# Optimization experiments

Hardware: AMD Instinct MI355X
Metric: run time of the kernel (lower is better)

The kernel has to match this reference:

```python
import jax, jax.numpy as jnp
import numpy as np

VOCAB, EMB, HID, NCLS = 50257, 48, 128, 2000
B, S = 512, 1024


def setup_inputs() -> dict:
    key = jax.random.key(0)
    ks = jax.random.split(key, 8)
    x = jax.random.randint(ks[0], (B, S), 0, VOCAB)
    emb_table = jax.random.normal(ks[1], (VOCAB, EMB), dtype=jnp.float32)
    emb_table = emb_table.at[0].set(0.0)  # padding_idx=0
    k_ih = 1.0 / np.sqrt(HID)
    w_ih = jax.random.uniform(ks[2], (4 * HID, EMB), minval=-k_ih, maxval=k_ih, dtype=jnp.float32)
    w_hh = jax.random.uniform(ks[3], (4 * HID, HID), minval=-k_ih, maxval=k_ih, dtype=jnp.float32)
    b_ih = jax.random.uniform(ks[4], (4 * HID,), minval=-k_ih, maxval=k_ih, dtype=jnp.float32)
    b_hh = jax.random.uniform(ks[5], (4 * HID,), minval=-k_ih, maxval=k_ih, dtype=jnp.float32)
    k_fc = 1.0 / np.sqrt(HID)
    w_fc = jax.random.uniform(ks[6], (NCLS, HID), minval=-k_fc, maxval=k_fc, dtype=jnp.float32)
    b_fc = jax.random.uniform(ks[7], (NCLS,), minval=-k_fc, maxval=k_fc, dtype=jnp.float32)
    return {"x": x, "emb_table": emb_table, "w_ih": w_ih, "w_hh": w_hh,
            "b_ih": b_ih, "b_hh": b_hh, "w_fc": w_fc, "b_fc": b_fc}


def _lstm_last_hidden(e, w_ih, w_hh, b_ih, b_hh):
    # e: [B, S, E]. Precompute input contributions for all timesteps (one big GEMM).
    xg = jnp.einsum('bse,ge->bsg', e, w_ih) + b_ih + b_hh  # [B, S, 4H]
    xg = jnp.transpose(xg, (1, 0, 2))                      # [S, B, 4H]
    Bn = e.shape[0]
    h0 = jnp.zeros((Bn, HID), e.dtype)
    c0 = jnp.zeros((Bn, HID), e.dtype)

    def step(carry, xg_t):
        h, c = carry
        g = xg_t + h @ w_hh.T                              # [B, 4H]
        i, f, gg, o = jnp.split(g, 4, axis=-1)             # PyTorch gate order i,f,g,o
        i = jax.nn.sigmoid(i)
        f = jax.nn.sigmoid(f)
        gg = jnp.tanh(gg)
        o = jax.nn.sigmoid(o)
        c = f * c + i * gg
        h = o * jnp.tanh(c)
        return (h, c), None

    (h_n, _), _ = jax.lax.scan(step, (h0, c0), xg)
    return h_n


def reference(x, emb_table, w_ih, w_hh, b_ih, b_hh, w_fc, b_fc):
    e = emb_table[x]                                       # [B, S, E] gather
    h_n = _lstm_last_hidden(e, w_ih, w_hh, b_ih, b_hh)     # [B, H]
    return h_n @ w_fc.T + b_fc                             # [B, NCLS]
```

## Files before the change

### kernel.cpp

```cpp
#include <hip/hip_runtime.h>

#define DI __device__ __forceinline__

typedef unsigned int uint;
typedef unsigned short ushort;
typedef _Float16 half2t __attribute__((ext_vector_type(2)));

#define VOCAB 50257
#define NEMB 48
#define HID 128
#define G4 512
#define NCLS 2000
#define BATCH 512
#define SEQ 1024

#if __has_builtin(__builtin_amdgcn_fdot2)
DI float fdot2(half2t a, half2t b, float c) { return __builtin_amdgcn_fdot2(a, b, c, false); }
#else
DI float fdot2(half2t a, half2t b, float c) { return c + (float)a.x * (float)b.x + (float)a.y * (float)b.y; }
#endif

DI float sigm(float x) {
  return __builtin_amdgcn_rcpf(1.0f + __builtin_amdgcn_exp2f(-1.4426950408889634f * x));
}
DI float tanhfast(float x) {
  return 1.0f - 2.0f * __builtin_amdgcn_rcpf(__builtin_amdgcn_exp2f(2.8853900817779268f * x) + 1.0f);
}

#define VROWS 32
__global__ __launch_bounds__(512) void build_P(
    const float* __restrict__ emb, const float* __restrict__ w_ih,
    const float* __restrict__ b_ih, const float* __restrict__ b_hh,
    _Float16* __restrict__ P)
{
  __shared__ __align__(16) float eL[VROWS][NEMB];
  const int tid = threadIdx.x;
  const int v0 = blockIdx.x * VROWS;
  int nrows = VOCAB - v0; if (nrows > VROWS) nrows = VROWS;

  for (int f = tid; f < nrows * NEMB; f += 512)
    eL[f / NEMB][f % NEMB] = emb[(size_t)v0 * NEMB + f];

  float w[NEMB];
  {
    const float* wr = w_ih + (size_t)tid * NEMB;
#pragma unroll
    for (int k = 0; k < NEMB; k++) w[k] = wr[k];
  }
  float bias = b_ih[tid] + b_hh[tid];
  __syncthreads();

  for (int v = 0; v < nrows; v++) {
    const float4* e4 = (const float4*)&eL[v][0];
    float a = bias;
#pragma unroll
    for (int k = 0; k < NEMB / 4; k++) {
      float4 e = e4[k];
      a += w[4 * k] * e.x + w[4 * k + 1] * e.y + w[4 * k + 2] * e.z + w[4 * k + 3] * e.w;
    }
    P[(size_t)(v0 + v) * G4 + tid] = (_Float16)a;
  }
}

template<bool USE_P>
__global__ __launch_bounds__(256, 2) void lstm_scan(
    const int* __restrict__ x, const float* __restrict__ emb,
    const float* __restrict__ w_ih, const float* __restrict__ w_hh,
    const float* __restrict__ b_ih, const float* __restrict__ b_hh,
    const _Float16* __restrict__ P, float* __restrict__ hout)
{
  __shared__ int tokL[SEQ];
  __shared__ __align__(16) _Float16 h16[HID];
  __shared__ float g32[G4];
  __shared__ __align__(8) half2t e16[2][NEMB / 2];

  const int tid = threadIdx.x;
  const int b = blockIdx.x;

  {
    const int* xp = x + (size_t)b * SEQ;
#pragma unroll
    for (int i = 0; i < SEQ / 256; i++) tokL[tid + 256 * i] = xp[tid + 256 * i];
  }

  half2t w0[HID / 2], w1[HID / 2];
  {
    const float4* wr0 = (const float4*)(w_hh + (size_t)tid * HID);
    const float4* wr1 = (const float4*)(w_hh + (size_t)(tid + 256) * HID);
#pragma unroll
    for (int k = 0; k < HID / 4; k++) {
      float4 a = wr0[k];
      half2t p; p.x = (_Float16)a.x; p.y = (_Float16)a.y; w0[2 * k] = p;
      p.x = (_Float16)a.z; p.y = (_Float16)a.w; w0[2 * k + 1] = p;
      float4 bv = wr1[k];
      p.x = (_Float16)bv.x; p.y = (_Float16)bv.y; w1[2 * k] = p;
      p.x = (_Float16)bv.z; p.y = (_Float16)bv.w; w1[2 * k + 1] = p;
    }
  }
  half2t wih0[NEMB / 2], wih1[NEMB / 2];
  float bias0 = 0.0f, bias1 = 0.0f;
  if (!USE_P) {
    const float* wr0 = w_ih + (size_t)tid * NEMB;
    const float* wr1 = w_ih + (size_t)(tid + 256) * NEMB;
#pragma unroll
    for (int k = 0; k < NEMB / 2; k++) {
      half2t p;
      p.x = (_Float16)wr0[2 * k]; p.y = (_Float16)wr0[2 * k + 1]; wih0[k] = p;
      p.x = (_Float16)wr1[2 * k]; p.y = (_Float16)wr1[2 * k + 1]; wih1[k] = p;
    }
    bias0 = b_ih[tid] + b_hh[tid];
    bias1 = b_ih[tid + 256] + b_hh[tid + 256];
  }
  if (tid < HID) h16[tid] = (_Float16)0.0f;
  __syncthreads();

  float c = 0.0f;
  _Float16 pa0{}, pa1{}, pb0{}, pb1{};
  float2 einfl = {0.0f, 0.0f};
  if (USE_P) {
    const _Float16* r0 = P + (size_t)tokL[0] * G4;
    const _Float16* r1 = P + (size_t)tokL[1] * G4;
    pa0 = r0[tid]; pa1 = r0[tid + 256];
    pb0 = r1[tid]; pb1 = r1[tid + 256];
  } else {
    if (tid < NEMB / 2) {
      float2 e0 = ((const float2*)(emb + (size_t)tokL[0] * NEMB))[tid];
      einfl    = ((const float2*)(emb + (size_t)tokL[1] * NEMB))[tid];
      half2t p; p.x = (_Float16)e0.x; p.y = (_Float16)e0.y;
      e16[0][tid] = p;
    }
  }
  __syncthreads();

#define STEP(t, par) do {                                                      \
    int tc = (t) + 2; if (tc > SEQ - 1) tc = SEQ - 1;                          \
    float xg0, xg1;                                                            \
    if (USE_P) {                                                               \
      xg0 = (float)((par) ? pb0 : pa0);                                        \
      xg1 = (float)((par) ? pb1 : pa1);                                        \
      const _Float16* rn = P + (size_t)tokL[tc] * G4;        \
      _Float16 n0 = rn[tid], n1 = rn[tid + 256];                               \
      if ((par) == 0) { pa0 = n0; pa1 = n1; } else { pb0 = n0; pb1 = n1; }     \
    } else {                                                                   \
      if (tid < NEMB / 2) {                                                    \
        half2t p; p.x = (_Float16)einfl.x; p.y = (_Float16)einfl.y;            \
        e16[((t) + 1) & 1][tid] = p;                                           \
        einfl = ((const float2*)(emb + (size_t)tokL[tc] * NEMB))[tid];         \
      }                                                                        \
      xg0 = bias0; xg1 = bias1;                                                \
      _Pragma("unroll")                                                        \
      for (int k = 0; k < NEMB / 2; k++) {                                     \
        xg0 = fdot2(wih0[k], e16[(par)][k], xg0);                              \
        xg1 = fdot2(wih1[k], e16[(par)][k], xg1);                              \
      }                                                                        \
    }                                                                          \
    const uint4* hv = (const uint4*)h16;                                       \
    float s0 = xg0, u0 = 0.0f, s1 = xg1, u1 = 0.0f;                            \
    _Pragma("unroll")                                                          \
    for (int kt = 0; kt < HID / 8; kt++) {                                     \
      uint4 hq = hv[kt];                                                       \
      half2t ha = __builtin_bit_cast(half2t, hq.x);                            \
      half2t hb = __builtin_bit_cast(half2t, hq.y);                            \
      half2t hc = __builtin_bit_cast(half2t, hq.z);                            \
      half2t hd = __builtin_bit_cast(half2t, hq.w);                            \
      s0 = fdot2(w0[4 * kt + 0], ha, s0);                                      \
      u0 = fdot2(w0[4 * kt + 1], hb, u0);                                      \
      s0 = fdot2(w0[4 * kt + 2], hc, s0);                                      \
      u0 = fdot2(w0[4 * kt + 3], hd, u0);                                      \
      s1 = fdot2(w1[4 * kt + 0], ha, s1);                                      \
      u1 = fdot2(w1[4 * kt + 1], hb, u1);                                      \
      s1 = fdot2(w1[4 * kt + 2], hc, s1);                                      \
      u1 = fdot2(w1[4 * kt + 3], hd, u1);                                      \
    }                                                                          \
    g32[tid] = s0 + u0;                                                        \
    g32[tid + 256] = s1 + u1;                                                  \
    __syncthreads();                                                           \
    if (tid < HID) {                                                           \
      float gi = g32[tid],           gf = g32[HID + tid];                      \
      float gc = g32[2 * HID + tid], go = g32[3 * HID + tid];                  \
      float fi = sigm(gi), ff = sigm(gf), gt = tanhfast(gc), fo = sigm(go);    \
      c = ff * c + fi * gt;                                                    \
      float hh = fo * tanhfast(c);                                             \
      h16[tid] = (_Float16)hh;                                                 \
      if ((t) == SEQ - 1) hout[(size_t)b * HID + tid] = hh;                    \
    }                                                                          \
    __syncthreads();                                                           \
  } while (0)

  for (int t = 0; t < SEQ; t += 2) { STEP(t, 0); STEP(t + 1, 1); }
#undef STEP
}

#define FCR 64
#define FCC 64
__global__ __launch_bounds__(256) void fc_kernel(
    const float* __restrict__ h, const float* __restrict__ w_fc,
    const float* __restrict__ b_fc, float* __restrict__ out)
{
  __shared__ float aT[HID][FCR];
  __shared__ float bT[HID][FCC];
  const int tid = threadIdx.x;
  const int r0 = blockIdx.y * FCR;
  const int c0 = blockIdx.x * FCC;

  for (int f = tid; f < FCR * (HID / 4); f += 256) {
    int row = f >> 5, q = f & 31;
    float4 v = ((const float4*)h)[(((size_t)(r0 + row)) << 5) + q];
    aT[4 * q + 0][row] = v.x; aT[4 * q + 1][row] = v.y;
    aT[4 * q + 2][row] = v.z; aT[4 * q + 3][row] = v.w;
    int wrow = c0 + row;
    float4 wv;
    if (wrow < NCLS) wv = ((const float4*)w_fc)[(((size_t)wrow) << 5) + q];
    else { wv.x = 0.f; wv.y = 0.f; wv.z = 0.f; wv.w = 0.f; }
    bT[4 * q + 0][row] = wv.x; bT[4 * q + 1][row] = wv.y;
    bT[4 * q + 2][row] = wv.z; bT[4 * q + 3][row] = wv.w;
  }
  __syncthreads();

  const int cr = tid & 15, rr = tid >> 4;
  float acc[4][4];
#pragma unroll
  for (int i = 0; i < 4; i++)
#pragma unroll
    for (int j = 0; j < 4; j++) acc[i][j] = 0.0f;

#pragma unroll 4
  for (int k = 0; k < HID; k++) {
    float4 av = *(const float4*)&aT[k][4 * rr];
    float4 bv = *(const float4*)&bT[k][4 * cr];
    float a[4] = {av.x, av.y, av.z, av.w};
    float bb[4] = {bv.x, bv.y, bv.z, bv.w};
#pragma unroll
    for (int i = 0; i < 4; i++)
#pragma unroll
      for (int j = 0; j < 4; j++) acc[i][j] += a[i] * bb[j];
  }

#pragma unroll
  for (int j = 0; j < 4; j++) {
    int cc = c0 + 4 * cr + j;
    if (cc < NCLS) {
      float bias = b_fc[cc];
#pragma unroll
      for (int i = 0; i < 4; i++)
        out[(size_t)(r0 + 4 * rr + i) * NCLS + cc] = acc[i][j] + bias;
    }
  }
}

extern "C" void kernel_launch(void* const* d_in, const int* in_sizes, int n_in,
                              void* d_out, int out_size, void* d_ws, size_t ws_size,
                              hipStream_t stream) {
  const int*   xx   = (const int*)d_in[0];
  const float* emb  = (const float*)d_in[1];
  const float* w_ih = (const float*)d_in[2];
  const float* w_hh = (const float*)d_in[3];
  const float* b_ih = (const float*)d_in[4];
  const float* b_hh = (const float*)d_in[5];
  const float* w_fc = (const float*)d_in[6];
  const float* b_fc = (const float*)d_in[7];
  float* out = (float*)d_out;

  const size_t pbytes = (size_t)VOCAB * G4 * sizeof(_Float16);
  const size_t palign = (pbytes + 255) & ~(size_t)255;
  const size_t hbytes = (size_t)BATCH * HID * sizeof(float);

  float* hout;
  if (ws_size >= palign + hbytes) {
    _Float16* P = (_Float16*)d_ws;
    hout = (float*)((char*)d_ws + palign);
    build_P<<<(VOCAB + VROWS - 1) / VROWS, 512, 0, stream>>>(emb, w_ih, b_ih, b_hh, P);
    lstm_scan<true><<<BATCH, 256, 0, stream>>>(xx, emb, w_ih, w_hh, b_ih, b_hh, P, hout);
  } else {
    hout = (float*)d_ws;
    lstm_scan<false><<<BATCH, 256, 0, stream>>>(xx, emb, w_ih, w_hh, b_ih, b_hh,
                                                (const _Float16*)nullptr, hout);
  }
  dim3 fcg((NCLS + FCC - 1) / FCC, BATCH / FCR);
  fc_kernel<<<fcg, 256, 0, stream>>>(hout, w_fc, b_fc, out);
}
```

Baseline: 1.003 ms.

## Remap LSTM scan to 128 threads with paired-lane gate dot products and DPP reduction

The recurrent scan now uses 128 threads per batch row. Each adjacent lane pair owns two hidden units and splits the K dimension in half, computing all four gates and combining the halves with a DPP swizzle. This removes the shared-memory gate buffer and one barrier per step, and double-buffers h so only one barrier remains per timestep. The precomputed input projection table is interleaved per hidden unit so each thread fetches its four gate values in one 8-byte load. In exchange, each block holds 256 half2 weight registers per thread at one block per CU-slot, which raises register pressure and lowers occupancy.

```diff
diff --git a/kernel.cpp b/kernel.cpp
--- a/kernel.cpp
+++ b/kernel.cpp
@@ -5,6 +5,7 @@
 typedef unsigned int uint;
 typedef unsigned short ushort;
 typedef _Float16 half2t __attribute__((ext_vector_type(2)));
+typedef _Float16 half4t __attribute__((ext_vector_type(4)));
 
 #define VOCAB 50257
 #define NEMB 48
@@ -27,13 +28,19 @@
   return 1.0f - 2.0f * __builtin_amdgcn_rcpf(__builtin_amdgcn_exp2f(2.8853900817779268f * x) + 1.0f);
 }
 
+DI float dppx1(float v) {
+  return __builtin_bit_cast(float,
+      __builtin_amdgcn_update_dpp(0, __builtin_bit_cast(int, v), 0xB1, 0xF, 0xF, true));
+}
+
 #define VROWS 32
 __global__ __launch_bounds__(512) void build_P(
     const float* __restrict__ emb, const float* __restrict__ w_ih,
     const float* __restrict__ b_ih, const float* __restrict__ b_hh,
-    _Float16* __restrict__ P)
+    ushort* __restrict__ P2)
 {
   __shared__ __align__(16) float eL[VROWS][NEMB];
+  __shared__ ushort pg[VROWS][G4];
   const int tid = threadIdx.x;
   const int v0 = blockIdx.x * VROWS;
   int nrows = VOCAB - v0; if (nrows > VROWS) nrows = VROWS;
@@ -41,11 +48,11 @@
   for (int f = tid; f < nrows * NEMB; f += 512)
     eL[f / NEMB][f % NEMB] = emb[(size_t)v0 * NEMB + f];
 
-  float w[NEMB];
+  float wv[NEMB];
   {
     const float* wr = w_ih + (size_t)tid * NEMB;
 #pragma unroll
-    for (int k = 0; k < NEMB; k++) w[k] = wr[k];
+    for (int k = 0; k < NEMB; k++) wv[k] = wr[k];
   }
   float bias = b_ih[tid] + b_hh[tid];
   __syncthreads();
@@ -56,134 +63,156 @@
 #pragma unroll
     for (int k = 0; k < NEMB / 4; k++) {
       float4 e = e4[k];
-      a += w[4 * k] * e.x + w[4 * k + 1] * e.y + w[4 * k + 2] * e.z + w[4 * k + 3] * e.w;
-    }
-    P[(size_t)(v0 + v) * G4 + tid] = (_Float16)a;
+      a += wv[4 * k] * e.x + wv[4 * k + 1] * e.y + wv[4 * k + 2] * e.z + wv[4 * k + 3] * e.w;
+    }
+    pg[v][tid] = __builtin_bit_cast(ushort, (_Float16)a);
+  }
+  __syncthreads();
+  for (int f = tid; f < nrows * (G4 / 4); f += 512) {
+    int v = f >> 7, u = f & 127;
+    uint2 pk;
+    pk.x = (uint)pg[v][u]       | ((uint)pg[v][u + 128] << 16);
+    pk.y = (uint)pg[v][u + 256] | ((uint)pg[v][u + 384] << 16);
+    ((uint2*)(P2 + (size_t)(v0 + v) * G4))[u] = pk;
   }
 }
 
 template<bool USE_P>
-__global__ __launch_bounds__(256, 2) void lstm_scan(
+__global__ __launch_bounds__(128, 1) void lstm_scan(
     const int* __restrict__ x, const float* __restrict__ emb,
     const float* __restrict__ w_ih, const float* __restrict__ w_hh,
     const float* __restrict__ b_ih, const float* __restrict__ b_hh,
-    const _Float16* __restrict__ P, float* __restrict__ hout)
+    const ushort* __restrict__ P2, float* __restrict__ hout)
 {
   __shared__ int tokL[SEQ];
-  __shared__ __align__(16) _Float16 h16[HID];
-  __shared__ float g32[G4];
+  __shared__ __align__(16) _Float16 h16[2][HID];
   __shared__ __align__(8) half2t e16[2][NEMB / 2];
 
   const int tid = threadIdx.x;
-  const int b = blockIdx.x;
+  const int b   = blockIdx.x;
+  const int sub = tid & 1;
+  const int u0  = tid & ~1;
 
   {
     const int* xp = x + (size_t)b * SEQ;
 #pragma unroll
-    for (int i = 0; i < SEQ / 256; i++) tokL[tid + 256 * i] = xp[tid + 256 * i];
-  }
-
-  half2t w0[HID / 2], w1[HID / 2];
-  {
-    const float4* wr0 = (const float4*)(w_hh + (size_t)tid * HID);
-    const float4* wr1 = (const float4*)(w_hh + (size_t)(tid + 256) * HID);
-#pragma unroll
-    for (int k = 0; k < HID / 4; k++) {
-      float4 a = wr0[k];
-      half2t p; p.x = (_Float16)a.x; p.y = (_Float16)a.y; w0[2 * k] = p;
-      p.x = (_Float16)a.z; p.y = (_Float16)a.w; w0[2 * k + 1] = p;
-      float4 bv = wr1[k];
-      p.x = (_Float16)bv.x; p.y = (_Float16)bv.y; w1[2 * k] = p;
-      p.x = (_Float16)bv.z; p.y = (_Float16)bv.w; w1[2 * k + 1] = p;
-    }
-  }
-  half2t wih0[NEMB / 2], wih1[NEMB / 2];
-  float bias0 = 0.0f, bias1 = 0.0f;
+    for (int i = 0; i < SEQ / 128; i++) tokL[tid + 128 * i] = xp[tid + 128 * i];
+  }
+
+  half2t w[8][32];
+#pragma unroll
+  for (int g = 0; g < 4; g++)
+#pragma unroll
+    for (int cc = 0; cc < 2; cc++) {
+      const float4* wr = (const float4*)(w_hh + (size_t)(g * HID + u0 + cc) * HID + 64 * sub);
+#pragma unroll
+      for (int k4 = 0; k4 < 16; k4++) {
+        float4 v = wr[k4];
+        half2t p;
+        p.x = (_Float16)v.x; p.y = (_Float16)v.y; w[2 * g + cc][2 * k4] = p;
+        p.x = (_Float16)v.z; p.y = (_Float16)v.w; w[2 * g + cc][2 * k4 + 1] = p;
+      }
+    }
+
+  half2t wih[4][NEMB / 2];
+  float biasg[4] = {0.f, 0.f, 0.f, 0.f};
   if (!USE_P) {
-    const float* wr0 = w_ih + (size_t)tid * NEMB;
-    const float* wr1 = w_ih + (size_t)(tid + 256) * NEMB;
-#pragma unroll
-    for (int k = 0; k < NEMB / 2; k++) {
-      half2t p;
-      p.x = (_Float16)wr0[2 * k]; p.y = (_Float16)wr0[2 * k + 1]; wih0[k] = p;
-      p.x = (_Float16)wr1[2 * k]; p.y = (_Float16)wr1[2 * k + 1]; wih1[k] = p;
-    }
-    bias0 = b_ih[tid] + b_hh[tid];
-    bias1 = b_ih[tid + 256] + b_hh[tid + 256];
-  }
-  if (tid < HID) h16[tid] = (_Float16)0.0f;
+#pragma unroll
+    for (int g = 0; g < 4; g++) {
+      const float* wr = w_ih + (size_t)(g * HID + tid) * NEMB;
+#pragma unroll
+      for (int k = 0; k < NEMB / 2; k++) {
+        half2t p; p.x = (_Float16)wr[2 * k]; p.y = (_Float16)wr[2 * k + 1];
+        wih[g][k] = p;
+      }
+      biasg[g] = b_ih[g * HID + tid] + b_hh[g * HID + tid];
+    }
+  }
+  h16[1][tid] = (_Float16)0.0f;
   __syncthreads();
 
   float c = 0.0f;
-  _Float16 pa0{}, pa1{}, pb0{}, pb1{};
+  uint2 pa{0, 0}, pb{0, 0};
   float2 einfl = {0.0f, 0.0f};
   if (USE_P) {
-    const _Float16* r0 = P + (size_t)tokL[0] * G4;
-    const _Float16* r1 = P + (size_t)tokL[1] * G4;
-    pa0 = r0[tid]; pa1 = r0[tid + 256];
-    pb0 = r1[tid]; pb1 = r1[tid + 256];
+    pa = ((const uint2*)(P2 + (size_t)tokL[0] * G4))[tid];
+    pb = ((const uint2*)(P2 + (size_t)tokL[1] * G4))[tid];
   } else {
     if (tid < NEMB / 2) {
       float2 e0 = ((const float2*)(emb + (size_t)tokL[0] * NEMB))[tid];
-      einfl    = ((const float2*)(emb + (size_t)tokL[1] * NEMB))[tid];
+      einfl     = ((const float2*)(emb + (size_t)tokL[1] * NEMB))[tid];
       half2t p; p.x = (_Float16)e0.x; p.y = (_Float16)e0.y;
       e16[0][tid] = p;
     }
-  }
-  __syncthreads();
+    __syncthreads();
+  }
 
 #define STEP(t, par) do {                                                      \
     int tc = (t) + 2; if (tc > SEQ - 1) tc = SEQ - 1;                          \
-    float xg0, xg1;                                                            \
+    int tn = tokL[tc];                                                         \
+    uint2 cur = (par) ? pb : pa;                                               \
     if (USE_P) {                                                               \
-      xg0 = (float)((par) ? pb0 : pa0);                                        \
-      xg1 = (float)((par) ? pb1 : pa1);                                        \
-      const _Float16* rn = P + (size_t)tokL[tc] * G4;        \
-      _Float16 n0 = rn[tid], n1 = rn[tid + 256];                               \
-      if ((par) == 0) { pa0 = n0; pa1 = n1; } else { pb0 = n0; pb1 = n1; }     \
+      uint2 nx = ((const uint2*)(P2 + (size_t)tn * G4))[tid];         \
+      if ((par) == 0) pa = nx; else pb = nx;                                   \
     } else {                                                                   \
       if (tid < NEMB / 2) {                                                    \
         half2t p; p.x = (_Float16)einfl.x; p.y = (_Float16)einfl.y;            \
         e16[((t) + 1) & 1][tid] = p;                                           \
-        einfl = ((const float2*)(emb + (size_t)tokL[tc] * NEMB))[tid];         \
+        einfl = ((const float2*)(emb + (size_t)tn * NEMB))[tid];               \
       }                                                                        \
-      xg0 = bias0; xg1 = bias1;                                                \
+    }                                                                          \
+    const uint4* hv = (const uint4*)((const _Float16*)h16[(par) ^ 1] + 64 * sub);\
+    float a0=0,a1=0,a2=0,a3=0,a4=0,a5=0,a6=0,a7=0;                             \
+    _Pragma("unroll")                                                          \
+    for (int q = 0; q < 8; q++) {                                              \
+      uint4 hq = hv[q];                                                        \
+      half2t h0 = __builtin_bit_cast(half2t, hq.x);                            \
+      half2t h1 = __builtin_bit_cast(half2t, hq.y);                            \
+      half2t h2 = __builtin_bit_cast(half2t, hq.z);                            \
+      half2t h3 = __builtin_bit_cast(half2t, hq.w);                            \
+      a0=fdot2(w[0][4*q],h0,a0); a1=fdot2(w[1][4*q],h0,a1);                    \
+      a2=fdot2(w[2][4*q],h0,a2); a3=fdot2(w[3][4*q],h0,a3);                    \
+      a4=fdot2(w[4][4*q],h0,a4); a5=fdot2(w[5][4*q],h0,a5);                    \
+      a6=fdot2(w[6][4*q],h0,a6); a7=fdot2(w[7][4*q],h0,a7);                    \
+      a0=fdot2(w[0][4*q+1],h1,a0); a1=fdot2(w[1][4*q+1],h1,a1);                \
+      a2=fdot2(w[2][4*q+1],h1,a2); a3=fdot2(w[3][4*q+1],h1,a3);                \
+      a4=fdot2(w[4][4*q+1],h1,a4); a5=fdot2(w[5][4*q+1],h1,a5);                \
+      a6=fdot2(w[6][4*q+1],h1,a6); a7=fdot2(w[7][4*q+1],h1,a7);                \
+      a0=fdot2(w[0][4*q+2],h2,a0); a1=fdot2(w[1][4*q+2],h2,a1);                \
+      a2=fdot2(w[2][4*q+2],h2,a2); a3=fdot2(w[3][4*q+2],h2,a3);                \
+      a4=fdot2(w[4][4*q+2],h2,a4); a5=fdot2(w[5][4*q+2],h2,a5);                \
+      a6=fdot2(w[6][4*q+2],h2,a6); a7=fdot2(w[7][4*q+2],h2,a7);                \
+      a0=fdot2(w[0][4*q+3],h3,a0); a1=fdot2(w[1][4*q+3],h3,a1);                \
+      a2=fdot2(w[2][4*q+3],h3,a2); a3=fdot2(w[3][4*q+3],h3,a3);                \
+      a4=fdot2(w[4][4*q+3],h3,a4); a5=fdot2(w[5][4*q+3],h3,a5);                \
+      a6=fdot2(w[6][4*q+3],h3,a6); a7=fdot2(w[7][4*q+3],h3,a7);                \
+    }                                                                          \
+    float f0 = a0 + dppx1(a0), f1 = a1 + dppx1(a1);                            \
+    float f2 = a2 + dppx1(a2), f3 = a3 + dppx1(a3);                            \
+    float f4 = a4 + dppx1(a4), f5 = a5 + dppx1(a5);                            \
+    float f6 = a6 + dppx1(a6), f7 = a7 + dppx1(a7);                            \
+    float xgi, xgf, xgg, xgo;                                                  \
+    if (USE_P) {                                                               \
+      half4t xv = __builtin_bit_cast(half4t, cur);                             \
+      xgi = (float)xv.x; xgf = (float)xv.y; xgg = (float)xv.z; xgo = (float)xv.w;\
+    } else {                                                                   \
+      xgi = biasg[0]; xgf = biasg[1]; xgg = biasg[2]; xgo = biasg[3];          \
       _Pragma("unroll")                                                        \
       for (int k = 0; k < NEMB / 2; k++) {                                     \
-        xg0 = fdot2(wih0[k], e16[(par)][k], xg0);                              \
-        xg1 = fdot2(wih1[k], e16[(par)][k], xg1);                              \
+        half2t ev = e16[(par)][k];                                             \
+        xgi = fdot2(wih[0][k], ev, xgi); xgf = fdot2(wih[1][k], ev, xgf);      \
+        xgg = fdot2(wih[2][k], ev, xgg); xgo = fdot2(wih[3][k], ev, xgo);      \
       }                                                                        \
     }                                                                          \
-    const uint4* hv = (const uint4*)h16;                                       \
-    float s0 = xg0, u0 = 0.0f, s1 = xg1, u1 = 0.0f;                            \
-    _Pragma("unroll")                                                          \
-    for (int kt = 0; kt < HID / 8; kt++) {                                     \
-      uint4 hq = hv[kt];                                                       \
-      half2t ha = __builtin_bit_cast(half2t, hq.x);                            \
-      half2t hb = __builtin_bit_cast(half2t, hq.y);                            \
-      half2t hc = __builtin_bit_cast(half2t, hq.z);                            \
-      half2t hd = __builtin_bit_cast(half2t, hq.w);                            \
-      s0 = fdot2(w0[4 * kt + 0], ha, s0);                                      \
-      u0 = fdot2(w0[4 * kt + 1], hb, u0);                                      \
-      s0 = fdot2(w0[4 * kt + 2], hc, s0);                                      \
-      u0 = fdot2(w0[4 * kt + 3], hd, u0);                                      \
-      s1 = fdot2(w1[4 * kt + 0], ha, s1);                                      \
-      u1 = fdot2(w1[4 * kt + 1], hb, u1);                                      \
-      s1 = fdot2(w1[4 * kt + 2], hc, s1);                                      \
-      u1 = fdot2(w1[4 * kt + 3], hd, u1);                                      \
-    }                                                                          \
-    g32[tid] = s0 + u0;                                                        \
-    g32[tid + 256] = s1 + u1;                                                  \
-    __syncthreads();                                                           \
-    if (tid < HID) {                                                           \
-      float gi = g32[tid],           gf = g32[HID + tid];                      \
-      float gc = g32[2 * HID + tid], go = g32[3 * HID + tid];                  \
-      float fi = sigm(gi), ff = sigm(gf), gt = tanhfast(gc), fo = sigm(go);    \
-      c = ff * c + fi * gt;                                                    \
-      float hh = fo * tanhfast(c);                                             \
-      h16[tid] = (_Float16)hh;                                                 \
-      if ((t) == SEQ - 1) hout[(size_t)b * HID + tid] = hh;                    \
-    }                                                                          \
+    float gi = (sub ? f1 : f0) + xgi;                                          \
+    float gf = (sub ? f3 : f2) + xgf;                                          \
+    float gc = (sub ? f5 : f4) + xgg;                                          \
+    float go = (sub ? f7 : f6) + xgo;                                          \
+    float fi = sigm(gi), ff = sigm(gf), gt = tanhfast(gc), fo = sigm(go);      \
+    c = ff * c + fi * gt;                                                      \
+    float hh = fo * tanhfast(c);                                               \
+    h16[(par)][tid] = (_Float16)hh;                                            \
+    if ((t) == SEQ - 1) hout[(size_t)b * HID + tid] = hh;                      \
     __syncthreads();                                                           \
   } while (0)
 
@@ -261,20 +290,20 @@
   const float* b_fc = (const float*)d_in[7];
   float* out = (float*)d_out;
 
-  const size_t pbytes = (size_t)VOCAB * G4 * sizeof(_Float16);
+  const size_t pbytes = (size_t)VOCAB * G4 * sizeof(ushort);
   const size_t palign = (pbytes + 255) & ~(size_t)255;
   const size_t hbytes = (size_t)BATCH * HID * sizeof(float);
 
   float* hout;
   if (ws_size >= palign + hbytes) {
-    _Float16* P = (_Float16*)d_ws;
+    ushort* P2 = (ushort*)d_ws;
     hout = (float*)((char*)d_ws + palign);
-    build_P<<<(VOCAB + VROWS - 1) / VROWS, 512, 0, stream>>>(emb, w_ih, b_ih, b_hh, P);
-    lstm_scan<true><<<BATCH, 256, 0, stream>>>(xx, emb, w_ih, w_hh, b_ih, b_hh, P, hout);
+    build_P<<<(VOCAB + VROWS - 1) / VROWS, 512, 0, stream>>>(emb, w_ih, b_ih, b_hh, P2);
+    lstm_scan<true><<<BATCH, 128, 0, stream>>>(xx, emb, w_ih, w_hh, b_ih, b_hh, P2, hout);
   } else {
     hout = (float*)d_ws;
-    lstm_scan<false><<<BATCH, 256, 0, stream>>>(xx, emb, w_ih, w_hh, b_ih, b_hh,
-                                                (const _Float16*)nullptr, hout);
+    lstm_scan<false><<<BATCH, 128, 0, stream>>>(xx, emb, w_ih, w_hh, b_ih, b_hh,
+                                                (const ushort*)nullptr, hout);
   }
   dim3 fcg((NCLS + FCC - 1) / FCC, BATCH / FCR);
   fc_kernel<<<fcg, 256, 0, stream>>>(hout, w_fc, b_fc, out);
```

Result: slower. 1.278 ms (+27.4%).
